# Optimization experiments

Hardware: AMD Instinct MI355X
Metric: run time of the kernel (lower is better)

## Reference

```python
import jax, jax.numpy as jnp
import numpy as np

B, S, IK, IV = 16, 2048, 3, 1
D = IK + IV          # input_size = 4
H = 256              # hidden_size
F = 512              # dim_feedforward
L = 2                # num_layers
EPS = 1e-5


def setup_inputs() -> dict:
    key = jax.random.key(0)
    ks = jax.random.split(key, 16)
    n = jax.random.normal
    inp = {
        'KEY': n(ks[0], (B, S, IK), jnp.float32),
        'VALUE': n(ks[1], (B, S, IV), jnp.float32),
        # per-layer kernel-attention projections (stacked on layer axis)
        'Wq': n(ks[2], (L, D, H), jnp.float32) * 0.1,
        'bq': jnp.zeros((L, H), jnp.float32),
        'Wk': n(ks[3], (L, D, H), jnp.float32) * 0.1,
        'bk': jnp.zeros((L, H), jnp.float32),
        'Wv': n(ks[4], (L, D, H), jnp.float32) * 0.1,
        'bv': jnp.zeros((L, H), jnp.float32),
        'Wo': n(ks[5], (L, H, D), jnp.float32) * 0.1,
        'bo': jnp.zeros((L, D), jnp.float32),
        'bw': jnp.ones((L,), jnp.float32),          # Gaussian kernel bandwidth
        # LayerNorm 1
        'g1': jnp.ones((L, D), jnp.float32),
        'be1': jnp.zeros((L, D), jnp.float32),
        # FFN
        'W1': n(ks[6], (L, D, F), jnp.float32) * 0.1,
        'b1': jnp.zeros((L, F), jnp.float32),
        'W2': n(ks[7], (L, F, D), jnp.float32) * 0.1,
        'b2': jnp.zeros((L, D), jnp.float32),
        # LayerNorm 2
        'g2': jnp.ones((L, D), jnp.float32),
        'be2': jnp.zeros((L, D), jnp.float32),
        # final fc: input_size -> input_v
        'Wfc': n(ks[8], (D, IV), jnp.float32) * 0.1,
        'bfc': jnp.zeros((IV,), jnp.float32),
    }
    return inp


def _layernorm(x, g, b):
    m = x.mean(-1, keepdims=True)
    v = ((x - m) ** 2).mean(-1, keepdims=True)
    return (x - m) * jax.lax.rsqrt(v + EPS) * g + b


def reference(KEY, VALUE, Wq, bq, Wk, bk, Wv, bv, Wo, bo, bw,
              g1, be1, W1, b1, W2, b2, g2, be2, Wfc, bfc):
    # positioning: concat coords and values -> [B, S, D]
    X = jnp.concatenate([KEY, VALUE], axis=-1)
    n_layers = Wq.shape[0]
    for i in range(n_layers):
        # Nadaraya-Watson Gaussian kernel attention (madsnn, type='nwd', kernel='gauss')
        Q = X @ Wq[i] + bq[i]                      # [B,S,H]
        K = X @ Wk[i] + bk[i]                      # [B,S,H]
        V = X @ Wv[i] + bv[i]                      # [B,S,H]
        # pairwise squared distances ||q-k||^2, [B,S,S]
        d2 = ((Q * Q).sum(-1)[:, :, None]
              + (K * K).sum(-1)[:, None, :]
              - 2.0 * jnp.einsum('bqh,bkh->bqk', Q, K))
        attn = jax.nn.softmax(-0.5 * d2 * (bw[i] ** 2), axis=-1)
        attn_out = jnp.einsum('bqk,bkh->bqh', attn, V) @ Wo[i] + bo[i]  # [B,S,D]
        # residual + LayerNorm + FFN + residual + LayerNorm (dropout = identity in eval)
        res = _layernorm(X + attn_out, g1[i], be1[i])
        ff = jax.nn.relu(res @ W1[i] + b1[i]) @ W2[i] + b2[i]
        X = _layernorm(res + ff, g2[i], be2[i])
    return X @ Wfc + bfc                            # [B,S,IV]
```

## Files before the change

### kernel.cpp

```cpp
#include <hip/hip_runtime.h>

#define BB 16
#define SS 2048
#define DD 4
#define HH 256
#define FF 512
#define NTOK (BB*SS)
#define EPSF 1e-5f


__device__ __forceinline__ float wred64(float v) {
#pragma unroll
  for (int m = 32; m > 0; m >>= 1) v += __shfl_xor(v, m, 64);
  return v;
}


__global__ __launch_bounds__(64) void prep_kernel(
    const float* __restrict__ Wq, const float* __restrict__ bq,
    const float* __restrict__ Wk, const float* __restrict__ bk,
    const float* __restrict__ Wv, const float* __restrict__ bv,
    const float* __restrict__ Wo, const float* __restrict__ bw,
    const float* __restrict__ W1, const float* __restrict__ b1,
    const float* __restrict__ W2,
    float* __restrict__ sm, float* __restrict__ w1t)
{
  const int i = blockIdx.x;
  const int lane = threadIdx.x;
  float m4[4][4] = {{0}}, gkk[4][4] = {{0}}, gqq[4][4] = {{0}}, wvo[4][4] = {{0}};
  float akk[4] = {0}, aqq[4] = {0}, bvo[4] = {0};
  float ck1 = 0.f, ck2 = 0.f, cq2 = 0.f;

  for (int h = lane; h < HH; h += 64) {
    float vq[4], vk[4], vv[4], wo4[4];
#pragma unroll
    for (int a = 0; a < 4; ++a) {
      vq[a] = Wq[(i*DD + a)*HH + h];
      vk[a] = Wk[(i*DD + a)*HH + h];
      vv[a] = Wv[(i*DD + a)*HH + h];
      wo4[a] = Wo[(i*HH + h)*DD + a];
    }
    const float bqh = bq[i*HH + h], bkh = bk[i*HH + h], bvh = bv[i*HH + h];
#pragma unroll
    for (int a = 0; a < 4; ++a) {
#pragma unroll
      for (int c = 0; c < 4; ++c) {
        m4[a][c]  = fmaf(vq[a], vk[c], m4[a][c]);
        gkk[a][c] = fmaf(vk[a], vk[c], gkk[a][c]);
        gqq[a][c] = fmaf(vq[a], vq[c], gqq[a][c]);
        wvo[a][c] = fmaf(vv[a], wo4[c], wvo[a][c]);
      }
      akk[a] = fmaf(vk[a], bqh - bkh, akk[a]);
      aqq[a] = fmaf(vq[a], bkh - bqh, aqq[a]);
      bvo[a] = fmaf(bvh, wo4[a], bvo[a]);
    }
    ck1 = fmaf(bqh, bkh, ck1);
    ck2 = fmaf(bkh, bkh, ck2);
    cq2 = fmaf(bqh, bqh, cq2);
  }
#pragma unroll
  for (int a = 0; a < 4; ++a) {
#pragma unroll
    for (int c = 0; c < 4; ++c) {
      m4[a][c]  = wred64(m4[a][c]);
      gkk[a][c] = wred64(gkk[a][c]);
      gqq[a][c] = wred64(gqq[a][c]);
      wvo[a][c] = wred64(wvo[a][c]);
    }
    akk[a] = wred64(akk[a]);
    aqq[a] = wred64(aqq[a]);
    bvo[a] = wred64(bvo[a]);
  }
  ck1 = wred64(ck1); ck2 = wred64(ck2); cq2 = wred64(cq2);

  if (lane == 0) {
    const float bwv = bw[i];
    const float bw2 = bwv * bwv;
    float* s = sm + i*128;
#pragma unroll
    for (int a = 0; a < 4; ++a) {
#pragma unroll
      for (int c = 0; c < 4; ++c) {
        s[a*4+c]      = bw2 * m4[a][c];
        s[16 + a*4+c] = -0.5f * bw2 * gkk[a][c];
        s[32 + a*4+c] = -0.5f * bw2 * gqq[a][c];
        s[48 + a*4+c] = wvo[a][c];
      }
      s[64+a] = bw2 * akk[a];
      s[68+a] = bw2 * aqq[a];
      s[72+a] = bvo[a];
    }
    s[76] = bw2 * (ck1 - 0.5f * ck2);
    s[77] = -0.5f * bw2 * cq2;
  }
  for (int f = lane; f < FF; f += 64) {
    float* rec = w1t + (i*FF + f)*12;
#pragma unroll
    for (int c = 0; c < 4; ++c) rec[c]   = W1[(i*DD + c)*FF + f];
#pragma unroll
    for (int c = 0; c < 4; ++c) rec[4+c] = W2[(i*FF + f)*DD + c];
    rec[8] = b1[i*FF + f];
    rec[9] = 0.f; rec[10] = 0.f; rec[11] = 0.f;
  }
}

__device__ __forceinline__ void compute_feat(const float x[4], const float* __restrict__ s,
                                             float* __restrict__ featrec)
{
  float P[4], VT[4], tk[4], tq[4];
#pragma unroll
  for (int a = 0; a < 4; ++a) {
    P[a]  = fmaf(s[a*4+3], x[3], fmaf(s[a*4+2], x[2], fmaf(s[a*4+1], x[1], s[a*4+0]*x[0])));
    tk[a] = fmaf(s[16+a*4+3], x[3], fmaf(s[16+a*4+2], x[2], fmaf(s[16+a*4+1], x[1], s[16+a*4+0]*x[0])));
    tq[a] = fmaf(s[32+a*4+3], x[3], fmaf(s[32+a*4+2], x[2], fmaf(s[32+a*4+1], x[1], s[32+a*4+0]*x[0])));
    VT[a] = s[72+a] + fmaf(s[48+3*4+a], x[3], fmaf(s[48+2*4+a], x[2], fmaf(s[48+1*4+a], x[1], s[48+0*4+a]*x[0])));
  }
  float R = s[76], C = s[77];
#pragma unroll
  for (int a = 0; a < 4; ++a) {
    R = fmaf(tk[a] + s[64+a], x[a], R);
    C = fmaf(tq[a] + s[68+a], x[a], C);
  }
  float4* fp = (float4*)featrec;
  fp[0] = make_float4(P[0], P[1], P[2], P[3]);
  fp[1] = make_float4(VT[0], VT[1], VT[2], VT[3]);
  fp[2] = make_float4(R, C, 0.f, 0.f);
}

__global__ __launch_bounds__(64) void f0_kernel(
    const float* __restrict__ KEY, const float* __restrict__ VALUE,
    const float* __restrict__ sm, float* __restrict__ X0, float* __restrict__ feat)
{
  const int gq = blockIdx.x*64 + threadIdx.x;
  float x[4];
  x[0] = KEY[gq*3 + 0];
  x[1] = KEY[gq*3 + 1];
  x[2] = KEY[gq*3 + 2];
  x[3] = VALUE[gq];
  *(float4*)(X0 + gq*4) = make_float4(x[0], x[1], x[2], x[3]);
  float fr[12];
  compute_feat(x, sm, fr);
  float4* fp = (float4*)(feat + (size_t)gq*12);
  fp[0] = ((float4*)fr)[0]; fp[1] = ((float4*)fr)[1]; fp[2] = ((float4*)fr)[2];
}

__global__ __launch_bounds__(256) void attn_kernel(
    const float* __restrict__ feat, const float* __restrict__ X,
    float* __restrict__ part)
{
  __shared__ float smem[6144];
  const int bid = blockIdx.x;
  const int qg = bid >> 2, kb = bid & 3;
  const int b = qg >> 3;
  const int qbase = (b << 11) + (qg & 7)*256;
  const int kbase = (b << 11) + kb*512;
  const int tid = threadIdx.x;
  const int lane = tid & 63, wave = tid >> 6;

  {
    const float4* src = (const float4*)(feat + (size_t)kbase*12);
    float4* dst = (float4*)smem;
    for (int t = tid; t < 1536; t += 256) dst[t] = src[t];
  }

  float xq[4][4], Cq[4], acc[4][5];
#pragma unroll
  for (int j = 0; j < 4; ++j) {
    const int gq = qbase + j*64 + lane;
    const float4 xv = *(const float4*)(X + gq*4);
    xq[j][0] = xv.x; xq[j][1] = xv.y; xq[j][2] = xv.z; xq[j][3] = xv.w;
    Cq[j] = feat[(size_t)gq*12 + 9];
#pragma unroll
    for (int c = 0; c < 5; ++c) acc[j][c] = 0.f;
  }
  __syncthreads();

  const float* kf = smem + wave*128*12;
#pragma unroll 2
  for (int k = 0; k < 128; ++k) {
    const float* kp = kf + k*12;
    const float4 P  = *(const float4*)kp;
    const float4 VT = *(const float4*)(kp + 4);
    const float R = kp[8];
#pragma unroll
    for (int j = 0; j < 4; ++j) {
      float l = fmaf(xq[j][3], P.w, fmaf(xq[j][2], P.z,
                fmaf(xq[j][1], P.y, fmaf(xq[j][0], P.x, R + Cq[j]))));
      const float e = __expf(l);
      acc[j][0] = fmaf(e, VT.x, acc[j][0]);
      acc[j][1] = fmaf(e, VT.y, acc[j][1]);
      acc[j][2] = fmaf(e, VT.z, acc[j][2]);
      acc[j][3] = fmaf(e, VT.w, acc[j][3]);
      acc[j][4] += e;
    }
  }
  __syncthreads();
  float* red = smem;
#pragma unroll
  for (int j = 0; j < 4; ++j) {
    float* rr = red + (wave*256 + j*64 + lane)*5;
#pragma unroll
    for (int c = 0; c < 5; ++c) rr[c] = acc[j][c];
  }
  __syncthreads();
  {
    float s[5];
#pragma unroll
    for (int c = 0; c < 5; ++c)
      s[c] = red[(0*256 + tid)*5 + c] + red[(1*256 + tid)*5 + c]
           + red[(2*256 + tid)*5 + c] + red[(3*256 + tid)*5 + c];
    const int gq = qbase + tid;
    float* pp = part + (size_t)gq*20 + kb*5;
#pragma unroll
    for (int c = 0; c < 5; ++c) pp[c] = s[c];
  }
}

__device__ __forceinline__ void ln4(const float t[4], const float* __restrict__ g,
                                    const float* __restrict__ b, float r[4])
{
  const float m = 0.25f*(t[0]+t[1]+t[2]+t[3]);
  const float d0 = t[0]-m, d1 = t[1]-m, d2 = t[2]-m, d3 = t[3]-m;
  const float v = 0.25f*(d0*d0 + d1*d1 + d2*d2 + d3*d3);
  const float sc = rsqrtf(v + EPSF);
  r[0] = fmaf(d0*sc, g[0], b[0]);
  r[1] = fmaf(d1*sc, g[1], b[1]);
  r[2] = fmaf(d2*sc, g[2], b[2]);
  r[3] = fmaf(d3*sc, g[3], b[3]);
}

__global__ __launch_bounds__(512) void combine_kernel(
    const float* __restrict__ part, const float* __restrict__ Xin,
    const float* __restrict__ w1t,
    const float* __restrict__ bo, const float* __restrict__ g1, const float* __restrict__ be1,
    const float* __restrict__ b2v, const float* __restrict__ g2, const float* __restrict__ be2,
    const float* __restrict__ smn,
    float* __restrict__ Xout, float* __restrict__ feat,
    const float* __restrict__ Wfc, const float* __restrict__ bfc,
    float* __restrict__ outp, int last)
{
  const int tok = threadIdx.x & 63, fc = threadIdx.x >> 6;
  const int gq = blockIdx.x*64 + tok;
  __shared__ float ress[64][4];
  __shared__ float redb[8][64][4];

  if (fc == 0) {
    const float* pp = part + (size_t)gq*20;
    float acc[5] = {0,0,0,0,0};
#pragma unroll
    for (int kb = 0; kb < 4; ++kb)
#pragma unroll
      for (int c = 0; c < 5; ++c) acc[c] += pp[kb*5 + c];
    const float inv = 1.0f / acc[4];
    const float4 xv = *(const float4*)(Xin + gq*4);
    float t[4];
    t[0] = xv.x + fmaf(acc[0], inv, bo[0]);
    t[1] = xv.y + fmaf(acc[1], inv, bo[1]);
    t[2] = xv.z + fmaf(acc[2], inv, bo[2]);
    t[3] = xv.w + fmaf(acc[3], inv, bo[3]);
    float r[4];
    ln4(t, g1, be1, r);
    ress[tok][0] = r[0]; ress[tok][1] = r[1]; ress[tok][2] = r[2]; ress[tok][3] = r[3];
  }
  __syncthreads();
  const float r0 = ress[tok][0], r1 = ress[tok][1], r2 = ress[tok][2], r3 = ress[tok][3];
  float fa[4] = {0,0,0,0};
  const float* wt = w1t + (size_t)fc*64*12;
#pragma unroll 4
  for (int f = 0; f < 64; ++f) {
    const float* rec = wt + f*12;
    const float4 w1r = *(const float4*)rec;
    const float4 w2r = *(const float4*)(rec + 4);
    const float b1f = rec[8];
    float h = fmaf(r3, w1r.w, fmaf(r2, w1r.z, fmaf(r1, w1r.y, fmaf(r0, w1r.x, b1f))));
    h = fmaxf(h, 0.f);
    fa[0] = fmaf(h, w2r.x, fa[0]);
    fa[1] = fmaf(h, w2r.y, fa[1]);
    fa[2] = fmaf(h, w2r.z, fa[2]);
    fa[3] = fmaf(h, w2r.w, fa[3]);
  }
  redb[fc][tok][0] = fa[0]; redb[fc][tok][1] = fa[1];
  redb[fc][tok][2] = fa[2]; redb[fc][tok][3] = fa[3];
  __syncthreads();
  if (fc == 0) {
    float ff[4];
#pragma unroll
    for (int c = 0; c < 4; ++c) {
      float s = b2v[c];
#pragma unroll
      for (int k = 0; k < 8; ++k) s += redb[k][tok][c];
      ff[c] = s;
    }
    float t2[4];
#pragma unroll
    for (int c = 0; c < 4; ++c) t2[c] = ress[tok][c] + ff[c];
    float y[4];
    ln4(t2, g2, be2, y);
    if (last) {
      outp[gq] = fmaf(y[3], Wfc[3], fmaf(y[2], Wfc[2], fmaf(y[1], Wfc[1], fmaf(y[0], Wfc[0], bfc[0]))));
    } else {
      *(float4*)(Xout + gq*4) = make_float4(y[0], y[1], y[2], y[3]);
      float fr[12];
      compute_feat(y, smn, fr);
      float4* fp = (float4*)(feat + (size_t)gq*12);
      fp[0] = ((float4*)fr)[0]; fp[1] = ((float4*)fr)[1]; fp[2] = ((float4*)fr)[2];
    }
  }
}

extern "C" void kernel_launch(void* const* d_in, const int* in_sizes, int n_in,
                              void* d_out, int out_size, void* d_ws, size_t ws_size,
                              hipStream_t stream)
{
  const float* KEY   = (const float*)d_in[0];
  const float* VALUE = (const float*)d_in[1];
  const float* Wq  = (const float*)d_in[2];
  const float* bq  = (const float*)d_in[3];
  const float* Wk  = (const float*)d_in[4];
  const float* bk  = (const float*)d_in[5];
  const float* Wv  = (const float*)d_in[6];
  const float* bv  = (const float*)d_in[7];
  const float* Wo  = (const float*)d_in[8];
  const float* bo  = (const float*)d_in[9];
  const float* bw  = (const float*)d_in[10];
  const float* g1  = (const float*)d_in[11];
  const float* be1 = (const float*)d_in[12];
  const float* W1  = (const float*)d_in[13];
  const float* b1  = (const float*)d_in[14];
  const float* W2  = (const float*)d_in[15];
  const float* b2  = (const float*)d_in[16];
  const float* g2  = (const float*)d_in[17];
  const float* be2 = (const float*)d_in[18];
  const float* Wfc = (const float*)d_in[19];
  const float* bfc = (const float*)d_in[20];
  float* out = (float*)d_out;

  float* w    = (float*)d_ws;
  float* sm   = w;
  float* w1t  = w + 256;
  float* feat = w + 12544;
  float* X0   = w + 405760;
  float* X1   = w + 536832;
  float* part = w + 667904;

  prep_kernel<<<2, 64, 0, stream>>>(Wq, bq, Wk, bk, Wv, bv, Wo, bw, W1, b1, W2, sm, w1t);
  f0_kernel<<<NTOK/64, 64, 0, stream>>>(KEY, VALUE, sm, X0, feat);

  attn_kernel<<<512, 256, 0, stream>>>(feat, X0, part);
  combine_kernel<<<NTOK/64, 512, 0, stream>>>(part, X0, w1t,
      bo, g1, be1, b2, g2, be2,
      sm + 128, X1, feat, Wfc, bfc, out, 0);

  attn_kernel<<<512, 256, 0, stream>>>(feat, X1, part);
  combine_kernel<<<NTOK/64, 512, 0, stream>>>(part, X1, w1t + FF*12,
      bo + 4, g1 + 4, be1 + 4, b2 + 4, g2 + 4, be2 + 4,
      sm, X0, feat, Wfc, bfc, out, 1);
}
```

Baseline: 199.7 us.

## Drop query-only softmax term, use exp2, and retile attention with per-wave partials

Removes the per-query constant C from the logits, since it cancels in the softmax normalisation. The bandwidth scale now folds in log2(e) so the inner loop can call the hardware exp2. The attention kernel is retiled so each thread owns 8 queries against a 256-key block, and the block-level LDS reduction is dropped. Each wave now writes its own partial stripe, and the combine kernel sums the 32 stripes. The aim is to cut per-element ALU work and synchronisation, at the cost of more partial-sum traffic through global memory and higher register pressure from 40 accumulators per thread.

Measured after the change: 198.4 us. Within noise of the previous version (-0.7%).

```diff
diff --git a/kernel.cpp b/kernel.cpp
--- a/kernel.cpp
+++ b/kernel.cpp
@@ -2,11 +2,15 @@
 
 #define BB 16
 #define SS 2048
-#define DD 4
-#define HH 256
+#define NTOK (BB*SS)
 #define FF 512
-#define NTOK (BB*SS)
 #define EPSF 1e-5f
+
+#if __has_builtin(__builtin_amdgcn_exp2f)
+#define EXP2F(x) __builtin_amdgcn_exp2f(x)
+#else
+#define EXP2F(x) exp2f(x)
+#endif
 
 
 __device__ __forceinline__ float wred64(float v) {
@@ -27,36 +31,33 @@
 {
   const int i = blockIdx.x;
   const int lane = threadIdx.x;
-  float m4[4][4] = {{0}}, gkk[4][4] = {{0}}, gqq[4][4] = {{0}}, wvo[4][4] = {{0}};
-  float akk[4] = {0}, aqq[4] = {0}, bvo[4] = {0};
-  float ck1 = 0.f, ck2 = 0.f, cq2 = 0.f;
-
-  for (int h = lane; h < HH; h += 64) {
+  float m4[4][4] = {{0}}, gkk[4][4] = {{0}}, wvo[4][4] = {{0}};
+  float akk[4] = {0}, bvo[4] = {0};
+  float ck1 = 0.f, ck2 = 0.f;
+
+  for (int h = lane; h < 256; h += 64) {
     float vq[4], vk[4], vv[4], wo4[4];
 #pragma unroll
     for (int a = 0; a < 4; ++a) {
-      vq[a] = Wq[(i*DD + a)*HH + h];
-      vk[a] = Wk[(i*DD + a)*HH + h];
-      vv[a] = Wv[(i*DD + a)*HH + h];
-      wo4[a] = Wo[(i*HH + h)*DD + a];
-    }
-    const float bqh = bq[i*HH + h], bkh = bk[i*HH + h], bvh = bv[i*HH + h];
+      vq[a]  = Wq[(i*4 + a)*256 + h];
+      vk[a]  = Wk[(i*4 + a)*256 + h];
+      vv[a]  = Wv[(i*4 + a)*256 + h];
+      wo4[a] = Wo[(i*256 + h)*4 + a];
+    }
+    const float bqh = bq[i*256 + h], bkh = bk[i*256 + h], bvh = bv[i*256 + h];
 #pragma unroll
     for (int a = 0; a < 4; ++a) {
 #pragma unroll
       for (int c = 0; c < 4; ++c) {
         m4[a][c]  = fmaf(vq[a], vk[c], m4[a][c]);
         gkk[a][c] = fmaf(vk[a], vk[c], gkk[a][c]);
-        gqq[a][c] = fmaf(vq[a], vq[c], gqq[a][c]);
         wvo[a][c] = fmaf(vv[a], wo4[c], wvo[a][c]);
       }
       akk[a] = fmaf(vk[a], bqh - bkh, akk[a]);
-      aqq[a] = fmaf(vq[a], bkh - bqh, aqq[a]);
       bvo[a] = fmaf(bvh, wo4[a], bvo[a]);
     }
     ck1 = fmaf(bqh, bkh, ck1);
     ck2 = fmaf(bkh, bkh, ck2);
-    cq2 = fmaf(bqh, bqh, cq2);
   }
 #pragma unroll
   for (int a = 0; a < 4; ++a) {
@@ -64,41 +65,36 @@
     for (int c = 0; c < 4; ++c) {
       m4[a][c]  = wred64(m4[a][c]);
       gkk[a][c] = wred64(gkk[a][c]);
-      gqq[a][c] = wred64(gqq[a][c]);
       wvo[a][c] = wred64(wvo[a][c]);
     }
     akk[a] = wred64(akk[a]);
-    aqq[a] = wred64(aqq[a]);
     bvo[a] = wred64(bvo[a]);
   }
-  ck1 = wred64(ck1); ck2 = wred64(ck2); cq2 = wred64(cq2);
+  ck1 = wred64(ck1); ck2 = wred64(ck2);
 
   if (lane == 0) {
     const float bwv = bw[i];
-    const float bw2 = bwv * bwv;
-    float* s = sm + i*128;
+    const float bw2 = bwv * bwv * 1.44269504088896f;
+    float* s = sm + i*64;
 #pragma unroll
     for (int a = 0; a < 4; ++a) {
 #pragma unroll
       for (int c = 0; c < 4; ++c) {
         s[a*4+c]      = bw2 * m4[a][c];
         s[16 + a*4+c] = -0.5f * bw2 * gkk[a][c];
-        s[32 + a*4+c] = -0.5f * bw2 * gqq[a][c];
-        s[48 + a*4+c] = wvo[a][c];
+        s[32 + a*4+c] = wvo[a][c];
       }
-      s[64+a] = bw2 * akk[a];
-      s[68+a] = bw2 * aqq[a];
-      s[72+a] = bvo[a];
-    }
-    s[76] = bw2 * (ck1 - 0.5f * ck2);
-    s[77] = -0.5f * bw2 * cq2;
+      s[48+a] = bw2 * akk[a];
+      s[52+a] = bvo[a];
+    }
+    s[56] = bw2 * (ck1 - 0.5f * ck2);
   }
   for (int f = lane; f < FF; f += 64) {
     float* rec = w1t + (i*FF + f)*12;
 #pragma unroll
-    for (int c = 0; c < 4; ++c) rec[c]   = W1[(i*DD + c)*FF + f];
-#pragma unroll
-    for (int c = 0; c < 4; ++c) rec[4+c] = W2[(i*FF + f)*DD + c];
+    for (int c = 0; c < 4; ++c) rec[c]   = W1[(i*4 + c)*FF + f];
+#pragma unroll
+    for (int c = 0; c < 4; ++c) rec[4+c] = W2[(i*FF + f)*4 + c];
     rec[8] = b1[i*FF + f];
     rec[9] = 0.f; rec[10] = 0.f; rec[11] = 0.f;
   }
@@ -107,37 +103,33 @@
 __device__ __forceinline__ void compute_feat(const float x[4], const float* __restrict__ s,
                                              float* __restrict__ featrec)
 {
-  float P[4], VT[4], tk[4], tq[4];
+  float P[4], VT[4], tk[4];
 #pragma unroll
   for (int a = 0; a < 4; ++a) {
     P[a]  = fmaf(s[a*4+3], x[3], fmaf(s[a*4+2], x[2], fmaf(s[a*4+1], x[1], s[a*4+0]*x[0])));
     tk[a] = fmaf(s[16+a*4+3], x[3], fmaf(s[16+a*4+2], x[2], fmaf(s[16+a*4+1], x[1], s[16+a*4+0]*x[0])));
-    tq[a] = fmaf(s[32+a*4+3], x[3], fmaf(s[32+a*4+2], x[2], fmaf(s[32+a*4+1], x[1], s[32+a*4+0]*x[0])));
-    VT[a] = s[72+a] + fmaf(s[48+3*4+a], x[3], fmaf(s[48+2*4+a], x[2], fmaf(s[48+1*4+a], x[1], s[48+0*4+a]*x[0])));
-  }
-  float R = s[76], C = s[77];
-#pragma unroll
-  for (int a = 0; a < 4; ++a) {
-    R = fmaf(tk[a] + s[64+a], x[a], R);
-    C = fmaf(tq[a] + s[68+a], x[a], C);
-  }
+    VT[a] = s[52+a] + fmaf(s[32+3*4+a], x[3], fmaf(s[32+2*4+a], x[2], fmaf(s[32+1*4+a], x[1], s[32+0*4+a]*x[0])));
+  }
+  float R = s[56];
+#pragma unroll
+  for (int a = 0; a < 4; ++a) R = fmaf(tk[a] + s[48+a], x[a], R);
   float4* fp = (float4*)featrec;
   fp[0] = make_float4(P[0], P[1], P[2], P[3]);
   fp[1] = make_float4(VT[0], VT[1], VT[2], VT[3]);
-  fp[2] = make_float4(R, C, 0.f, 0.f);
-}
-
-__global__ __launch_bounds__(64) void f0_kernel(
+  fp[2] = make_float4(R, 0.f, 0.f, 0.f);
+}
+
+__global__ __launch_bounds__(256) void f0_kernel(
     const float* __restrict__ KEY, const float* __restrict__ VALUE,
     const float* __restrict__ sm, float* __restrict__ X0, float* __restrict__ feat)
 {
-  const int gq = blockIdx.x*64 + threadIdx.x;
+  const int gq = blockIdx.x*256 + threadIdx.x;
   float x[4];
   x[0] = KEY[gq*3 + 0];
   x[1] = KEY[gq*3 + 1];
   x[2] = KEY[gq*3 + 2];
   x[3] = VALUE[gq];
-  *(float4*)(X0 + gq*4) = make_float4(x[0], x[1], x[2], x[3]);
+  *(float4*)(X0 + (size_t)gq*4) = make_float4(x[0], x[1], x[2], x[3]);
   float fr[12];
   compute_feat(x, sm, fr);
   float4* fp = (float4*)(feat + (size_t)gq*12);
@@ -148,45 +140,46 @@
     const float* __restrict__ feat, const float* __restrict__ X,
     float* __restrict__ part)
 {
-  __shared__ float smem[6144];
+  __shared__ float kbuf[256*12];
   const int bid = blockIdx.x;
-  const int qg = bid >> 2, kb = bid & 3;
-  const int b = qg >> 3;
-  const int qbase = (b << 11) + (qg & 7)*256;
-  const int kbase = (b << 11) + kb*512;
+  const int b = bid >> 5;
+  const int r = bid & 31;
+  const int qg = r >> 3, kb = r & 7;
+  const int qbase = (b << 11) + (qg << 9);
+  const int kbase = (b << 11) + (kb << 8);
   const int tid = threadIdx.x;
   const int lane = tid & 63, wave = tid >> 6;
 
   {
     const float4* src = (const float4*)(feat + (size_t)kbase*12);
-    float4* dst = (float4*)smem;
-    for (int t = tid; t < 1536; t += 256) dst[t] = src[t];
-  }
-
-  float xq[4][4], Cq[4], acc[4][5];
-#pragma unroll
-  for (int j = 0; j < 4; ++j) {
-    const int gq = qbase + j*64 + lane;
-    const float4 xv = *(const float4*)(X + gq*4);
+    float4* dst = (float4*)kbuf;
+    dst[tid] = src[tid];
+    dst[tid + 256] = src[tid + 256];
+    dst[tid + 512] = src[tid + 512];
+  }
+
+  float xq[8][4], acc[8][5];
+#pragma unroll
+  for (int j = 0; j < 8; ++j) {
+    const float4 xv = *(const float4*)(X + (size_t)(qbase + j*64 + lane)*4);
     xq[j][0] = xv.x; xq[j][1] = xv.y; xq[j][2] = xv.z; xq[j][3] = xv.w;
-    Cq[j] = feat[(size_t)gq*12 + 9];
 #pragma unroll
     for (int c = 0; c < 5; ++c) acc[j][c] = 0.f;
   }
   __syncthreads();
 
-  const float* kf = smem + wave*128*12;
+  const float* kf = kbuf + wave*64*12;
 #pragma unroll 2
-  for (int k = 0; k < 128; ++k) {
+  for (int k = 0; k < 64; ++k) {
     const float* kp = kf + k*12;
     const float4 P  = *(const float4*)kp;
     const float4 VT = *(const float4*)(kp + 4);
     const float R = kp[8];
 #pragma unroll
-    for (int j = 0; j < 4; ++j) {
+    for (int j = 0; j < 8; ++j) {
       float l = fmaf(xq[j][3], P.w, fmaf(xq[j][2], P.z,
-                fmaf(xq[j][1], P.y, fmaf(xq[j][0], P.x, R + Cq[j]))));
-      const float e = __expf(l);
+                fmaf(xq[j][1], P.y, fmaf(xq[j][0], P.x, R))));
+      const float e = EXP2F(l);
       acc[j][0] = fmaf(e, VT.x, acc[j][0]);
       acc[j][1] = fmaf(e, VT.y, acc[j][1]);
       acc[j][2] = fmaf(e, VT.z, acc[j][2]);
@@ -194,25 +187,14 @@
       acc[j][4] += e;
     }
   }
-  __syncthreads();
-  float* red = smem;
-#pragma unroll
-  for (int j = 0; j < 4; ++j) {
-    float* rr = red + (wave*256 + j*64 + lane)*5;
-#pragma unroll
-    for (int c = 0; c < 5; ++c) rr[c] = acc[j][c];
-  }
-  __syncthreads();
-  {
-    float s[5];
-#pragma unroll
-    for (int c = 0; c < 5; ++c)
-      s[c] = red[(0*256 + tid)*5 + c] + red[(1*256 + tid)*5 + c]
-           + red[(2*256 + tid)*5 + c] + red[(3*256 + tid)*5 + c];
-    const int gq = qbase + tid;
-    float* pp = part + (size_t)gq*20 + kb*5;
-#pragma unroll
-    for (int c = 0; c < 5; ++c) pp[c] = s[c];
+
+  const int stripe = (kb << 2) + wave;
+  float* pb = part + (size_t)stripe * NTOK * 5;
+#pragma unroll
+  for (int j = 0; j < 8; ++j) {
+    float* pp = pb + (size_t)(qbase + j*64 + lane)*5;
+    pp[0] = acc[j][0]; pp[1] = acc[j][1]; pp[2] = acc[j][2];
+    pp[3] = acc[j][3]; pp[4] = acc[j][4];
   }
 }
 
@@ -241,18 +223,31 @@
 {
   const int tok = threadIdx.x & 63, fc = threadIdx.x >> 6;
   const int gq = blockIdx.x*64 + tok;
+  __shared__ float redp[8][64][5];
   __shared__ float ress[64][4];
-  __shared__ float redb[8][64][4];
+  __shared__ float redf[8][64][4];
+
+  {
+    float a5[5] = {0,0,0,0,0};
+#pragma unroll
+    for (int s = 0; s < 4; ++s) {
+      const float* pp = part + ((size_t)(fc*4 + s)*NTOK + gq)*5;
+#pragma unroll
+      for (int c = 0; c < 5; ++c) a5[c] += pp[c];
+    }
+#pragma unroll
+    for (int c = 0; c < 5; ++c) redp[fc][tok][c] = a5[c];
+  }
+  __syncthreads();
 
   if (fc == 0) {
-    const float* pp = part + (size_t)gq*20;
     float acc[5] = {0,0,0,0,0};
 #pragma unroll
-    for (int kb = 0; kb < 4; ++kb)
-#pragma unroll
-      for (int c = 0; c < 5; ++c) acc[c] += pp[kb*5 + c];
+    for (int k = 0; k < 8; ++k)
+#pragma unroll
+      for (int c = 0; c < 5; ++c) acc[c] += redp[k][tok][c];
     const float inv = 1.0f / acc[4];
-    const float4 xv = *(const float4*)(Xin + gq*4);
+    const float4 xv = *(const float4*)(Xin + (size_t)gq*4);
     float t[4];
     t[0] = xv.x + fmaf(acc[0], inv, bo[0]);
     t[1] = xv.y + fmaf(acc[1], inv, bo[1]);
@@ -263,6 +258,7 @@
     ress[tok][0] = r[0]; ress[tok][1] = r[1]; ress[tok][2] = r[2]; ress[tok][3] = r[3];
   }
   __syncthreads();
+
   const float r0 = ress[tok][0], r1 = ress[tok][1], r2 = ress[tok][2], r3 = ress[tok][3];
   float fa[4] = {0,0,0,0};
   const float* wt = w1t + (size_t)fc*64*12;
@@ -279,27 +275,25 @@
     fa[2] = fmaf(h, w2r.z, fa[2]);
     fa[3] = fmaf(h, w2r.w, fa[3]);
   }
-  redb[fc][tok][0] = fa[0]; redb[fc][tok][1] = fa[1];
-  redb[fc][tok][2] = fa[2]; redb[fc][tok][3] = fa[3];
+  redf[fc][tok][0] = fa[0]; redf[fc][tok][1] = fa[1];
+  redf[fc][tok][2] = fa[2]; redf[fc][tok][3] = fa[3];
   __syncthreads();
+
   if (fc == 0) {
-    float ff[4];
+    float t2[4];
 #pragma unroll
     for (int c = 0; c < 4; ++c) {
       float s = b2v[c];
 #pragma unroll
-      for (int k = 0; k < 8; ++k) s += redb[k][tok][c];
-      ff[c] = s;
-    }
-    float t2[4];
-#pragma unroll
-    for (int c = 0; c < 4; ++c) t2[c] = ress[tok][c] + ff[c];
+      for (int k = 0; k < 8; ++k) s += redf[k][tok][c];
+      t2[c] = ress[tok][c] + s;
+    }
     float y[4];
     ln4(t2, g2, be2, y);
     if (last) {
       outp[gq] = fmaf(y[3], Wfc[3], fmaf(y[2], Wfc[2], fmaf(y[1], Wfc[1], fmaf(y[0], Wfc[0], bfc[0]))));
     } else {
-      *(float4*)(Xout + gq*4) = make_float4(y[0], y[1], y[2], y[3]);
+      *(float4*)(Xout + (size_t)gq*4) = make_float4(y[0], y[1], y[2], y[3]);
       float fr[12];
       compute_feat(y, smn, fr);
       float4* fp = (float4*)(feat + (size_t)gq*12);
@@ -337,22 +331,22 @@
 
   float* w    = (float*)d_ws;
   float* sm   = w;
-  float* w1t  = w + 256;
-  float* feat = w + 12544;
-  float* X0   = w + 405760;
-  float* X1   = w + 536832;
-  float* part = w + 667904;
+  float* w1t  = w + 128;
+  float* feat = w + 12416;
+  float* X0   = w + 405632;
+  float* X1   = w + 536704;
+  float* part = w + 667776;
 
   prep_kernel<<<2, 64, 0, stream>>>(Wq, bq, Wk, bk, Wv, bv, Wo, bw, W1, b1, W2, sm, w1t);
-  f0_kernel<<<NTOK/64, 64, 0, stream>>>(KEY, VALUE, sm, X0, feat);
+  f0_kernel<<<128, 256, 0, stream>>>(KEY, VALUE, sm, X0, feat);
 
   attn_kernel<<<512, 256, 0, stream>>>(feat, X0, part);
-  combine_kernel<<<NTOK/64, 512, 0, stream>>>(part, X0, w1t,
+  combine_kernel<<<512, 512, 0, stream>>>(part, X0, w1t,
       bo, g1, be1, b2, g2, be2,
-      sm + 128, X1, feat, Wfc, bfc, out, 0);
+      sm + 64, X1, feat, Wfc, bfc, out, 0);
 
   attn_kernel<<<512, 256, 0, stream>>>(feat, X1, part);
-  combine_kernel<<<NTOK/64, 512, 0, stream>>>(part, X1, w1t + FF*12,
+  combine_kernel<<<512, 512, 0, stream>>>(part, X1, w1t + FF*12,
       bo + 4, g1 + 4, be1 + 4, b2 + 4, g2 + 4, be2 + 4,
       sm, X0, feat, Wfc, bfc, out, 1);
 }
```
